# Optimization experiments

Hardware: AMD Instinct MI355X
Metric: run time of the kernel (lower is better)

The kernel has to match this reference:

```python
import jax, jax.numpy as jnp
import numpy as np

DIM = 256
N_STATE = 8
DT_RANK = 16  # ceil(dim/16)
D_CONV = 4
HIDDEN = 128  # dim * rank_ratio
EPS = 1e-6


def rmsnorm(x, w):
    # matches torch: x / (||x||_2 / sqrt(d) + eps) * w
    norm = jnp.sqrt(jnp.sum(x * x, axis=-1, keepdims=True))
    return x / (norm / np.sqrt(x.shape[-1]) + EPS) * w


def dwconv1d(x, w, b, pad_l, pad_r):
    # x: (b, l, c); w: (c, 1, k) depthwise
    out = jax.lax.conv_general_dilated(
        x.transpose(0, 2, 1), w, window_strides=(1,),
        padding=[(pad_l, pad_r)], dimension_numbers=('NCH', 'OIH', 'NCH'),
        feature_group_count=w.shape[0])
    return (out + b[None, :, None]).transpose(0, 2, 1)


def selective_scan(x, delta, A, Bm, Cm, D):
    # x, delta: (b,l,d); A: (d,n); Bm, Cm: (b,l,n); D: (d,)
    dA = jnp.exp(delta[..., None] * A)                     # (b,l,d,n)
    dBx = (delta * x)[..., None] * Bm[:, :, None, :]       # (b,l,d,n)

    def step(h, inp):
        dA_t, dBx_t, C_t = inp
        h = dA_t * h + dBx_t                               # (b,d,n)
        y = jnp.einsum('bdn,bn->bd', h, C_t)
        return h, y

    h0 = jnp.zeros((x.shape[0],) + A.shape, dtype=x.dtype)
    _, ys = jax.lax.scan(step, h0,
                         (dA.transpose(1, 0, 2, 3), dBx.transpose(1, 0, 2, 3),
                          Cm.transpose(1, 0, 2)))
    return ys.transpose(1, 0, 2) + x * D                   # (b,l,d)


def mamba_branch(x, ctx, conv_w, conv_b, xproj_w, dtproj_w, dtproj_b, A_log, D):
    xc = jax.nn.silu(dwconv1d(x, conv_w, conv_b, D_CONV - 1, 0))  # causal conv
    x_dbl = ctx @ xproj_w.T                                  # (b,l,r+2n)
    dt, Bm, Cm = jnp.split(x_dbl, [DT_RANK, DT_RANK + N_STATE], axis=-1)
    delta = jax.nn.softplus(dt @ dtproj_w.T + dtproj_b)
    A = -jnp.exp(A_log)
    return selective_scan(xc, delta, A, Bm, Cm, D)


def setup_inputs() -> dict:
    key = jax.random.key(0)
    ks = jax.random.split(key, 24)
    B, L, D = 4, 64 * 64, DIM
    s = 0.02
    A_log_init = jnp.log(jnp.broadcast_to(jnp.arange(1, N_STATE + 1, dtype=jnp.float32), (D, N_STATE)))
    dt_bias = jnp.full((D,), jnp.log(jnp.expm1(0.01)), dtype=jnp.float32)
    inp = {
        'x0': jax.random.normal(ks[0], (B, L, D), jnp.float32),
        'x1': jax.random.normal(ks[1], (B, L, D), jnp.float32),
        'w_norm0': jnp.ones((D,), jnp.float32),
        'w_norm1': jnp.ones((D,), jnp.float32),
        'in_proj_w': jax.random.normal(ks[2], (2 * D, D), jnp.float32) * s,
        'conv_w_f': jax.random.normal(ks[3], (D, 1, D_CONV), jnp.float32) * 0.3,
        'conv_b_f': jnp.zeros((D,), jnp.float32),
        'xproj_w_f': jax.random.normal(ks[4], (DT_RANK + 2 * N_STATE, D), jnp.float32) * s,
        'dtproj_w_f': jax.random.normal(ks[5], (D, DT_RANK), jnp.float32) * 0.1,
        'dtproj_b_f': dt_bias,
        'A_log_f': A_log_init,
        'D_f': jnp.ones((D,), jnp.float32),
        'conv_w_bw': jax.random.normal(ks[6], (D, 1, D_CONV), jnp.float32) * 0.3,
        'conv_b_bw': jnp.zeros((D,), jnp.float32),
        'xproj_w_bw': jax.random.normal(ks[7], (DT_RANK + 2 * N_STATE, D), jnp.float32) * s,
        'dtproj_w_bw': jax.random.normal(ks[8], (D, DT_RANK), jnp.float32) * 0.1,
        'dtproj_b_bw': dt_bias,
        'A_log_bw': A_log_init,
        'D_bw': jnp.ones((D,), jnp.float32),
        'norm_y_w': jnp.ones((D,), jnp.float32),
        'out_proj_w': jax.random.normal(ks[9], (D, D), jnp.float32) * s,
        'fc1_w': jax.random.normal(ks[10], (HIDDEN, D), jnp.float32) * s,
        'dw_w': jax.random.normal(ks[11], (HIDDEN, 1, 3), jnp.float32) * 0.3,
        'dw_b': jnp.zeros((HIDDEN,), jnp.float32),
        'fc2_w': jax.random.normal(ks[12], (D, HIDDEN), jnp.float32) * s,
    }
    return inp


def reference(x0, x1, w_norm0, w_norm1, in_proj_w, conv_w_f, conv_b_f, xproj_w_f,
              dtproj_w_f, dtproj_b_f, A_log_f, D_f, conv_w_bw, conv_b_bw,
              xproj_w_bw, dtproj_w_bw, dtproj_b_bw, A_log_bw, D_bw, norm_y_w,
              out_proj_w, fc1_w, dw_w, dw_b, fc2_w):
    residual = x0
    h0 = rmsnorm(x0, w_norm0)
    h1 = rmsnorm(x1, w_norm1)
    # cross-Mamba: main stream x0 -> x,z; extra_emb x1 -> dt/B/C
    xz = h0 @ in_proj_w.T
    xin, z = jnp.split(xz, 2, axis=-1)
    y_f = mamba_branch(xin, h1, conv_w_f, conv_b_f, xproj_w_f, dtproj_w_f,
                       dtproj_b_f, A_log_f, D_f)
    y_b = jnp.flip(mamba_branch(jnp.flip(xin, 1), jnp.flip(h1, 1), conv_w_bw,
                                conv_b_bw, xproj_w_bw, dtproj_w_bw, dtproj_b_bw,
                                A_log_bw, D_bw), 1)
    y = (y_f + y_b) * 0.5          # if_devide_out=True (bidirectional)
    y = rmsnorm(y, norm_y_w)       # use_norm=True
    y = y * jax.nn.silu(z)
    x = y @ out_proj_w.T + residual
    # LowRankFeedForward (dropout = identity at eval)
    m = x @ fc1_w.T
    m = jax.nn.silu(dwconv1d(m, dw_w, dw_b, 1, 1))
    m = m @ fc2_w.T
    return x + m
```

## Files before the change

kernel.cpp:

```cpp
#include <hip/hip_runtime.h>
#include <math.h>
#include <cstddef>

#define BB 4
#define LL 4096
#define DD 256
#define NST 8
#define RANK 16
#define HID 128
#define BL (BB*LL)
#define BLD ((size_t)BL*DD)
#define CH 128
#define CLEN 32
#define XZS 512

typedef __bf16 bf16x8 __attribute__((ext_vector_type(8)));
typedef float  f32x4  __attribute__((ext_vector_type(4)));

__device__ __forceinline__ float siluf(float x){ return x / (1.f + __expf(-x)); }
__device__ __forceinline__ float softplus_fast(float x){
  float r = __logf(1.f + __expf(x));
  return x > 15.f ? x : r;
}
__device__ __forceinline__ unsigned short f2bf(float x){
  union { float f; unsigned u; } v; v.f = x;
  unsigned r = v.u + 0x7fffu + ((v.u >> 16) & 1u);
  return (unsigned short)(r >> 16);
}
__device__ __forceinline__ float bf2f(unsigned short u){
  union { unsigned u32; float f; } c; c.u32 = ((unsigned)u) << 16;
  return c.f;
}

__global__ __launch_bounds__(64) void rms_kernel(
    const float* __restrict__ x0, const float* __restrict__ w0, unsigned short* __restrict__ o0b,
    const float* __restrict__ x1, const float* __restrict__ w1, unsigned short* __restrict__ o1b)
{
  const float* x; const float* w; unsigned short* o;
  if (blockIdx.y == 0){ x = x0; w = w0; o = o0b; } else { x = x1; w = w1; o = o1b; }
  size_t tok = blockIdx.x;
  int lane = threadIdx.x;
  float4 v = ((const float4*)(x + tok*DD))[lane];
  float s = v.x*v.x + v.y*v.y + v.z*v.z + v.w*v.w;
  #pragma unroll
  for (int m = 1; m < 64; m <<= 1) s += __shfl_xor(s, m, 64);
  float scale = 1.f / (sqrtf(s) * (1.f/16.f) + 1e-6f);
  float4 wv = ((const float4*)w)[lane];
  ushort4 r;
  r.x = f2bf(v.x*scale*wv.x); r.y = f2bf(v.y*scale*wv.y);
  r.z = f2bf(v.z*scale*wv.z); r.w = f2bf(v.w*scale*wv.w);
  ((ushort4*)(o + tok*DD))[lane] = r;
}

__global__ __launch_bounds__(256) void cvt_all_kernel(
    const float* __restrict__ ip,
    const float* __restrict__ s0, const float* __restrict__ s1,
    const float* __restrict__ s2, const float* __restrict__ s3,
    const float* __restrict__ s4,
    unsigned short* __restrict__ d1, unsigned short* __restrict__ d2)
{
  int i = blockIdx.x*256 + threadIdx.x;
  if (i < 131072){ d1[i] = f2bf(ip[i]); return; }
  int j = i - 131072;
  if (j >= 147456) return;
  float v;
  if (j < 8192)        v = s0[j];
  else if (j < 16384)  v = s1[j - 8192];
  else if (j < 81920)  v = s2[j - 16384];
  else if (j < 114688) v = s3[j - 81920];
  else                 v = s4[j - 114688];
  d2[j] = f2bf(v);
}

template<int EPI>
__global__ __launch_bounds__(256) void gemm_mfma128(
    const unsigned short* __restrict__ A, const unsigned short* __restrict__ Bw,
    float* __restrict__ C, const float* __restrict__ Add,
    unsigned short* __restrict__ Cb, int M, int ldc, int K)
{
  constexpr int BM = 128, BN = 128, BK = 32, PAD = 8;
  __shared__ __align__(16) unsigned short As[BM][BK+PAD];
  __shared__ __align__(16) unsigned short Bs[BN][BK+PAD];
  int tid  = threadIdx.x;
  int row0 = blockIdx.x * BM;
  int col0 = blockIdx.y * BN;
  int wave = tid >> 6, lane = tid & 63;
  int wm = (wave >> 1) * 64, wn = (wave & 1) * 64;
  int lm = lane & 15, kq = lane >> 4;

  f32x4 acc[4][4];
  #pragma unroll
  for (int i = 0; i < 4; i++)
    #pragma unroll
    for (int j = 0; j < 4; j++) acc[i][j] = (f32x4){0.f,0.f,0.f,0.f};

  for (int k0 = 0; k0 < K; k0 += BK){
    #pragma unroll
    for (int e = tid; e < BM*4; e += 256){
      int r = e >> 2, c8 = (e & 3) * 8;
      *(int4*)&As[r][c8] = *(const int4*)&A[(size_t)(row0 + r)*K + k0 + c8];
    }
    #pragma unroll
    for (int e = tid; e < BN*4; e += 256){
      int r = e >> 2, c8 = (e & 3) * 8;
      *(int4*)&Bs[r][c8] = *(const int4*)&Bw[(size_t)(col0 + r)*K + k0 + c8];
    }
    __syncthreads();
    bf16x8 af[4], bfv[4];
    #pragma unroll
    for (int i = 0; i < 4; i++) af[i]  = *(const bf16x8*)&As[wm + i*16 + lm][kq*8];
    #pragma unroll
    for (int j = 0; j < 4; j++) bfv[j] = *(const bf16x8*)&Bs[wn + j*16 + lm][kq*8];
    #pragma unroll
    for (int i = 0; i < 4; i++)
      #pragma unroll
      for (int j = 0; j < 4; j++)
        acc[i][j] = __builtin_amdgcn_mfma_f32_16x16x32_bf16(af[i], bfv[j], acc[i][j], 0, 0, 0);
    __syncthreads();
  }

  #pragma unroll
  for (int i = 0; i < 4; i++){
    int rbase = row0 + wm + i*16 + kq*4;
    #pragma unroll
    for (int j = 0; j < 4; j++){
      int col = col0 + wn + j*16 + lm;
      #pragma unroll
      for (int r = 0; r < 4; r++){
        size_t idx = (size_t)(rbase + r)*ldc + col;
        float v = acc[i][j][r];
        if constexpr (EPI == 1 || EPI == 2) v += Add[idx];
        if constexpr (EPI != 3) C[idx] = v;
        if constexpr (EPI == 1 || EPI == 3) Cb[idx] = f2bf(v);
      }
    }
  }
}

template<int EPI>
__global__ __launch_bounds__(256) void gemm_mfma(
    const unsigned short* __restrict__ A, const unsigned short* __restrict__ Bw,
    float* __restrict__ C, const float* __restrict__ Add,
    unsigned short* __restrict__ Cb, int M, int ldc, int K)
{
  constexpr int BK = 32, PAD = 8;
  __shared__ __align__(16) unsigned short As[64][BK+PAD];
  __shared__ __align__(16) unsigned short Bs[64][BK+PAD];
  int tid  = threadIdx.x;
  int row0 = blockIdx.x * 64;
  int col0 = blockIdx.y * 64;
  int wave = tid >> 6, lane = tid & 63;
  int wm = (wave >> 1) * 32, wn = (wave & 1) * 32;
  int lm = lane & 15, kq = lane >> 4;
  int sr = tid >> 2, sc8 = (tid & 3) * 8;

  f32x4 acc[2][2];
  #pragma unroll
  for (int i = 0; i < 2; i++)
    #pragma unroll
    for (int j = 0; j < 2; j++) acc[i][j] = (f32x4){0.f,0.f,0.f,0.f};

  for (int k0 = 0; k0 < K; k0 += BK){
    *(int4*)&As[sr][sc8] = *(const int4*)&A [(size_t)(row0 + sr)*K + k0 + sc8];
    *(int4*)&Bs[sr][sc8] = *(const int4*)&Bw[(size_t)(col0 + sr)*K + k0 + sc8];
    __syncthreads();
    bf16x8 af[2], bfv[2];
    #pragma unroll
    for (int i = 0; i < 2; i++) af[i]  = *(const bf16x8*)&As[wm + i*16 + lm][kq*8];
    #pragma unroll
    for (int j = 0; j < 2; j++) bfv[j] = *(const bf16x8*)&Bs[wn + j*16 + lm][kq*8];
    #pragma unroll
    for (int i = 0; i < 2; i++)
      #pragma unroll
      for (int j = 0; j < 2; j++)
        acc[i][j] = __builtin_amdgcn_mfma_f32_16x16x32_bf16(af[i], bfv[j], acc[i][j], 0, 0, 0);
    __syncthreads();
  }

  #pragma unroll
  for (int i = 0; i < 2; i++){
    int rbase = row0 + wm + i*16 + kq*4;
    #pragma unroll
    for (int j = 0; j < 2; j++){
      int col = col0 + wn + j*16 + lm;
      #pragma unroll
      for (int r = 0; r < 4; r++){
        size_t idx = (size_t)(rbase + r)*ldc + col;
        float v = acc[i][j][r];
        if constexpr (EPI == 1 || EPI == 2) v += Add[idx];
        if constexpr (EPI != 3) C[idx] = v;
        if constexpr (EPI == 1 || EPI == 3) Cb[idx] = f2bf(v);
      }
    }
  }
}

__global__ __launch_bounds__(256) void front_kernel(
    const unsigned short* __restrict__ xz,
    const float* __restrict__ xd,
    const float* __restrict__ cwf, const float* __restrict__ cbf,
    const float* __restrict__ cwb, const float* __restrict__ cbb,
    const float* __restrict__ dtwf, const float* __restrict__ dtbf,
    const float* __restrict__ dtwb, const float* __restrict__ dtbb,
    const float* __restrict__ Alogf, const float* __restrict__ Alogb,
    unsigned int* __restrict__ xde,
    float* __restrict__ P, float* __restrict__ Hout)
{
  int chunk = blockIdx.x, b = blockIdx.y, dir = blockIdx.z;
  int s0 = chunk*CLEN;
  int d  = threadIdx.x;

  __shared__ float sdt[CLEN][16];
  __shared__ float sB [CLEN][8];
  {
    #pragma unroll
    for (int e = threadIdx.x; e < CLEN*16; e += 256){
      int lt = e >> 4, col = e & 15;
      int pos = s0 + lt;
      int row = dir ? (LL-1-pos) : pos;
      sdt[lt][col] = xd[((size_t)b*LL + row)*64 + dir*32 + col];
    }
    {
      int e = threadIdx.x;
      int lt = e >> 3, col = e & 7;
      int pos = s0 + lt;
      int row = dir ? (LL-1-pos) : pos;
      sB[lt][col] = xd[((size_t)b*LL + row)*64 + dir*32 + 16 + col];
    }
  }
  __syncthreads();

  float4 cw = ((const float4*)(dir ? cwb : cwf))[d];
  float cb  = (dir ? cbb : cbf)[d];
  const float* dtw = (dir ? dtwb : dtwf) + d*RANK;
  float4 w0 = ((const float4*)dtw)[0], w1 = ((const float4*)dtw)[1];
  float4 w2 = ((const float4*)dtw)[2], w3 = ((const float4*)dtw)[3];
  float dtb = (dir ? dtbb : dtbf)[d];

  const unsigned short* xp = xz + (size_t)b*LL*XZS + d;
  #define LDX(pos) ((pos) >= 0 ? bf2f(xp[(size_t)(dir ? (LL-1-(pos)) : (pos))*XZS]) : 0.f)

  float a0, a1, a2, a3;
  a1 = LDX(s0-3); a2 = LDX(s0-2); a3 = LDX(s0-1);

  unsigned packX[CLEN];
  const int U = 8;
  float px[U];
  #pragma unroll
  for (int u = 0; u < U; u++) px[u] = LDX(s0+u);

  for (int g = 0; g < CLEN; g += U){
    float nx[U];
    if (g + U < CLEN){
      #pragma unroll
      for (int u = 0; u < U; u++) nx[u] = LDX(s0+g+U+u);
    }
    #pragma unroll
    for (int u = 0; u < U; u++){
      int i = g + u;
      a0 = a1; a1 = a2; a2 = a3; a3 = px[u];
      float xc = cb;
      xc = fmaf(cw.x, a0, xc); xc = fmaf(cw.y, a1, xc);
      xc = fmaf(cw.z, a2, xc); xc = fmaf(cw.w, a3, xc);
      xc = siluf(xc);
      const float* dt = &sdt[i][0];
      float de = dtb;
      de = fmaf(dt[0],w0.x, fmaf(dt[1],w0.y, fmaf(dt[2],w0.z, fmaf(dt[3],w0.w, de))));
      de = fmaf(dt[4],w1.x, fmaf(dt[5],w1.y, fmaf(dt[6],w1.z, fmaf(dt[7],w1.w, de))));
      de = fmaf(dt[8],w2.x, fmaf(dt[9],w2.y, fmaf(dt[10],w2.z, fmaf(dt[11],w2.w, de))));
      de = fmaf(dt[12],w3.x, fmaf(dt[13],w3.y, fmaf(dt[14],w3.z, fmaf(dt[15],w3.w, de))));
      de = softplus_fast(de);
      unsigned pk = (unsigned)f2bf(xc) | ((unsigned)f2bf(de) << 16);
      packX[i] = pk;
      xde[((size_t)(dir*BB + b)*LL + (s0+i))*DD + d] = pk;
    }
    if (g + U < CLEN){
      #pragma unroll
      for (int u = 0; u < U; u++) px[u] = nx[u];
    }
  }
  #undef LDX

  const float* Alog = dir ? Alogb : Alogf;
  float A[NST];
  #pragma unroll
  for (int n = 0; n < NST; n++) A[n] = -__expf(Alog[d*NST + n]);
  float h[NST];
  #pragma unroll
  for (int n = 0; n < NST; n++) h[n] = 0.f;
  float S = 0.f;
  #pragma unroll
  for (int t = 0; t < CLEN; t++){
    unsigned pk = packX[t];
    float xc = bf2f((unsigned short)(pk & 0xffffu));
    float de = bf2f((unsigned short)(pk >> 16));
    S += de;
    float dux = de * xc;
    const float* Bv = &sB[t][0];
    h[0] = fmaf(__expf(de*A[0]), h[0], dux*Bv[0]);
    h[1] = fmaf(__expf(de*A[1]), h[1], dux*Bv[1]);
    h[2] = fmaf(__expf(de*A[2]), h[2], dux*Bv[2]);
    h[3] = fmaf(__expf(de*A[3]), h[3], dux*Bv[3]);
    h[4] = fmaf(__expf(de*A[4]), h[4], dux*Bv[4]);
    h[5] = fmaf(__expf(de*A[5]), h[5], dux*Bv[5]);
    h[6] = fmaf(__expf(de*A[6]), h[6], dux*Bv[6]);
    h[7] = fmaf(__expf(de*A[7]), h[7], dux*Bv[7]);
  }
  size_t ob = ((((size_t)dir*CH + chunk)*BB + b)*DD + d)*NST;
  float4 p0, p1h, h0v, h1v;
  p0.x = __expf(A[0]*S); p0.y = __expf(A[1]*S); p0.z = __expf(A[2]*S); p0.w = __expf(A[3]*S);
  p1h.x= __expf(A[4]*S); p1h.y= __expf(A[5]*S); p1h.z= __expf(A[6]*S); p1h.w= __expf(A[7]*S);
  h0v.x=h[0]; h0v.y=h[1]; h0v.z=h[2]; h0v.w=h[3];
  h1v.x=h[4]; h1v.y=h[5]; h1v.z=h[6]; h1v.w=h[7];
  *(float4*)&P[ob]      = p0;  *(float4*)&P[ob+4]    = p1h;
  *(float4*)&Hout[ob]   = h0v; *(float4*)&Hout[ob+4] = h1v;
}

__global__ __launch_bounds__(64) void scan_p2(
    const float* P, const float* __restrict__ Hout, float* Hin)
{
  int tid = blockIdx.x*64 + threadIdx.x;
  int dir = tid >> 13;
  int b   = (tid >> 11) & 3;
  int dn  = tid & 2047;
  const size_t stride = (size_t)BB*2048;
  size_t idx0 = (((size_t)dir*CH)*BB + b)*2048 + dn;

  const int U = 8;
  float pp[U], hh[U];
  #pragma unroll
  for (int u = 0; u < U; u++){
    pp[u] = P[idx0 + u*stride];
    hh[u] = Hout[idx0 + u*stride];
  }
  float h = 0.f;
  for (int c0 = 0; c0 < CH; c0 += U){
    float np[U], nh[U];
    if (c0 + U < CH){
      #pragma unroll
      for (int u = 0; u < U; u++){
        np[u] = P[idx0 + (size_t)(c0+U+u)*stride];
        nh[u] = Hout[idx0 + (size_t)(c0+U+u)*stride];
      }
    }
    #pragma unroll
    for (int u = 0; u < U; u++){
      Hin[idx0 + (size_t)(c0+u)*stride] = h;
      h = fmaf(pp[u], h, hh[u]);
    }
    if (c0 + U < CH){
      #pragma unroll
      for (int u = 0; u < U; u++){ pp[u] = np[u]; hh[u] = nh[u]; }
    }
  }
}

__global__ __launch_bounds__(256) void scan_p3(
    const unsigned int* __restrict__ xde,
    const float* __restrict__ xd,
    const float* __restrict__ Alogf, const float* __restrict__ Alogb,
    const float* __restrict__ Dfp, const float* __restrict__ Dbp,
    const float* Hin,
    unsigned short* __restrict__ yf, unsigned short* __restrict__ yb)
{
  int chunk = blockIdx.x, b = blockIdx.y, dir = blockIdx.z;
  const float* Alog = dir ? Alogb : Alogf;
  int d = threadIdx.x;
  int base = chunk*CLEN;

  __shared__ float sBC[CLEN*16];
  {
    #pragma unroll
    for (int e = threadIdx.x; e < CLEN*16; e += 256){
      int lt = e >> 4, col = e & 15;
      int pos = base + lt;
      int row = dir ? (LL-1-pos) : pos;
      sBC[e] = xd[((size_t)b*LL + row)*64 + dir*32 + 16 + col];
    }
  }
  __syncthreads();

  float A[NST];
  #pragma unroll
  for (int n = 0; n < NST; n++) A[n] = -__expf(Alog[d*NST + n]);
  float Dd = (dir ? Dbp : Dfp)[d];

  float h[NST];
  {
    size_t ib = ((((size_t)dir*CH + chunk)*BB + b)*DD + d)*NST;
    float4 a0 = *(const float4*)&Hin[ib];
    float4 a1 = *(const float4*)&Hin[ib+4];
    h[0]=a0.x; h[1]=a0.y; h[2]=a0.z; h[3]=a0.w;
    h[4]=a1.x; h[5]=a1.y; h[6]=a1.z; h[7]=a1.w;
  }

  const unsigned int* xdep = xde + ((size_t)(dir*BB + b)*LL + base)*DD + d;
  unsigned short* yp = (dir ? yb : yf) + ((size_t)b*LL + base)*DD + d;

  const int U = 8;
  unsigned int pk[U];
  #pragma unroll
  for (int u = 0; u < U; u++) pk[u] = xdep[(size_t)u*DD];

  for (int t0 = 0; t0 < CLEN; t0 += U){
    unsigned int nk[U];
    if (t0 + U < CLEN){
      #pragma unroll
      for (int u = 0; u < U; u++) nk[u] = xdep[(size_t)(t0+U+u)*DD];
    }
    #pragma unroll
    for (int u = 0; u < U; u++){
      int t = t0 + u;
      float xc = bf2f((unsigned short)(pk[u] & 0xffffu));
      float de = bf2f((unsigned short)(pk[u] >> 16));
      float dux = de * xc;
      const float4 Bv0 = *(const float4*)&sBC[t*16 + 0];
      const float4 Bv1 = *(const float4*)&sBC[t*16 + 4];
      const float4 Cv0 = *(const float4*)&sBC[t*16 + 8];
      const float4 Cv1 = *(const float4*)&sBC[t*16 + 12];
      float acc = xc * Dd;
      h[0] = fmaf(__expf(de*A[0]), h[0], dux*Bv0.x); acc = fmaf(h[0], Cv0.x, acc);
      h[1] = fmaf(__expf(de*A[1]), h[1], dux*Bv0.y); acc = fmaf(h[1], Cv0.y, acc);
      h[2] = fmaf(__expf(de*A[2]), h[2], dux*Bv0.z); acc = fmaf(h[2], Cv0.z, acc);
      h[3] = fmaf(__expf(de*A[3]), h[3], dux*Bv0.w); acc = fmaf(h[3], Cv0.w, acc);
      h[4] = fmaf(__expf(de*A[4]), h[4], dux*Bv1.x); acc = fmaf(h[4], Cv1.x, acc);
      h[5] = fmaf(__expf(de*A[5]), h[5], dux*Bv1.y); acc = fmaf(h[5], Cv1.y, acc);
      h[6] = fmaf(__expf(de*A[6]), h[6], dux*Bv1.z); acc = fmaf(h[6], Cv1.z, acc);
      h[7] = fmaf(__expf(de*A[7]), h[7], dux*Bv1.w); acc = fmaf(h[7], Cv1.w, acc);
      yp[(size_t)t*DD] = f2bf(acc);
    }
    if (t0 + U < CLEN){
      #pragma unroll
      for (int u = 0; u < U; u++) pk[u] = nk[u];
    }
  }
}

__global__ __launch_bounds__(64) void combine_kernel(
    const unsigned short* __restrict__ yf, const unsigned short* __restrict__ yb,
    const unsigned short* __restrict__ xz, const float* __restrict__ wn,
    unsigned short* __restrict__ outb)
{
  size_t tok = blockIdx.x;
  int b = (int)(tok / LL), t = (int)(tok % LL);
  int lane = threadIdx.x;
  ushort4 au = ((const ushort4*)(yf + tok*DD))[lane];
  ushort4 cu = ((const ushort4*)(yb + ((size_t)b*LL + (LL-1-t))*DD))[lane];
  float4 v;
  v.x=(bf2f(au.x)+bf2f(cu.x))*0.5f; v.y=(bf2f(au.y)+bf2f(cu.y))*0.5f;
  v.z=(bf2f(au.z)+bf2f(cu.z))*0.5f; v.w=(bf2f(au.w)+bf2f(cu.w))*0.5f;
  float s = v.x*v.x + v.y*v.y + v.z*v.z + v.w*v.w;
  #pragma unroll
  for (int m = 1; m < 64; m <<= 1) s += __shfl_xor(s, m, 64);
  float scale = 1.f / (sqrtf(s)*(1.f/16.f) + 1e-6f);
  float4 wv = ((const float4*)wn)[lane];
  ushort4 zv = *(const ushort4*)&xz[tok*XZS + 256 + lane*4];
  ushort4 r;
  r.x = f2bf(v.x*scale*wv.x*siluf(bf2f(zv.x)));
  r.y = f2bf(v.y*scale*wv.y*siluf(bf2f(zv.y)));
  r.z = f2bf(v.z*scale*wv.z*siluf(bf2f(zv.z)));
  r.w = f2bf(v.w*scale*wv.w*siluf(bf2f(zv.w)));
  ((ushort4*)(outb + tok*DD))[lane] = r;
}

__global__ __launch_bounds__(256) void dwconv3_kernel(
    const float* __restrict__ m, const float* __restrict__ w,
    const float* __restrict__ bi, unsigned short* __restrict__ o)
{
  size_t gid = (size_t)blockIdx.x*256 + threadIdx.x;
  int c = (int)(gid % HID);
  int tok = (int)(gid / HID);
  int b = tok / LL, t = tok % LL;
  float acc = bi[c];
  #pragma unroll
  for (int k = 0; k < 3; k++){
    int tt = t - 1 + k;
    if (tt >= 0 && tt < LL)
      acc = fmaf(w[c*3 + k], m[((size_t)b*LL + tt)*HID + c], acc);
  }
  o[gid] = f2bf(siluf(acc));
}

extern "C" void kernel_launch(void* const* d_in, const int* in_sizes, int n_in,
                              void* d_out, int out_size, void* d_ws, size_t ws_size,
                              hipStream_t stream)
{
  const float* x0        = (const float*)d_in[0];
  const float* x1        = (const float*)d_in[1];
  const float* w_norm0   = (const float*)d_in[2];
  const float* w_norm1   = (const float*)d_in[3];
  const float* in_proj_w = (const float*)d_in[4];
  const float* conv_w_f  = (const float*)d_in[5];
  const float* conv_b_f  = (const float*)d_in[6];
  const float* xproj_w_f = (const float*)d_in[7];
  const float* dtproj_w_f= (const float*)d_in[8];
  const float* dtproj_b_f= (const float*)d_in[9];
  const float* A_log_f   = (const float*)d_in[10];
  const float* D_f       = (const float*)d_in[11];
  const float* conv_w_bw = (const float*)d_in[12];
  const float* conv_b_bw = (const float*)d_in[13];
  const float* xproj_w_bw= (const float*)d_in[14];
  const float* dtproj_w_bw=(const float*)d_in[15];
  const float* dtproj_b_bw=(const float*)d_in[16];
  const float* A_log_bw  = (const float*)d_in[17];
  const float* D_bw      = (const float*)d_in[18];
  const float* norm_y_w  = (const float*)d_in[19];
  const float* out_proj_w= (const float*)d_in[20];
  const float* fc1_w     = (const float*)d_in[21];
  const float* dw_w      = (const float*)d_in[22];
  const float* dw_b      = (const float*)d_in[23];
  const float* fc2_w     = (const float*)d_in[24];
  float* out = (float*)d_out;
  float* ws  = (float*)d_ws;

  float* r0 = ws + 0*BLD;
  float* r1 = ws + 1*BLD;
  float* r2 = ws + 2*BLD;
  float* r3 = ws + 3*BLD;
  float* r4 = ws + 4*BLD;
  float* r5 = ws + 5*BLD;
  float* r6 = ws + 6*BLD;
  float* r7 = ws + 7*BLD;

  unsigned short* h0b   = (unsigned short*)r0;
  unsigned short* h1b   = (unsigned short*)r1;
  unsigned short* xz_b  = (unsigned short*)r2;
  float*          xd    = r3;
  unsigned int*   xde   = (unsigned int*)r4;
  unsigned short* wbuf1 = (unsigned short*)r6;
  unsigned short* yfb   = (unsigned short*)r0;
  unsigned short* ybb   = (unsigned short*)r1;
  const size_t CARRY = (size_t)2*CH*BB*DD*NST;
  float* Pbuf = r6;
  float* Hout = r6 + CARRY;
  float* Hin  = Pbuf;
  unsigned short* ycomb_b = (unsigned short*)r3;
  unsigned short* wbuf2   = (unsigned short*)r7;
  unsigned short* wb_xp   = wbuf2;
  unsigned short* wb_out  = wbuf2 + 16384;
  unsigned short* wb_fc1  = wbuf2 + 81920;
  unsigned short* wb_fc2  = wbuf2 + 114688;
  unsigned short* xb      = wbuf2 + 147456;
  float*          m1      = r4;
  unsigned short* m2b     = (unsigned short*)r5;

  cvt_all_kernel<<<dim3(1088), 256, 0, stream>>>(
      in_proj_w, xproj_w_f, xproj_w_bw, out_proj_w, fc1_w, fc2_w, wbuf1, wbuf2);

  rms_kernel<<<dim3(BL,2), 64, 0, stream>>>(x0, w_norm0, h0b, x1, w_norm1, h1b);

  gemm_mfma128<3><<<dim3(BL/128, 4), 256, 0, stream>>>(
      h0b, wbuf1, nullptr, nullptr, xz_b, BL, XZS, 256);

  gemm_mfma<0><<<dim3(BL/64, 1), 256, 0, stream>>>(
      h1b, wb_xp, xd, nullptr, nullptr, BL, 64, 256);

  front_kernel<<<dim3(CH, BB, 2), 256, 0, stream>>>(
      xz_b, xd, conv_w_f, conv_b_f, conv_w_bw, conv_b_bw,
      dtproj_w_f, dtproj_b_f, dtproj_w_bw, dtproj_b_bw,
      A_log_f, A_log_bw, xde, Pbuf, Hout);

  scan_p2<<<dim3(256), 64, 0, stream>>>(Pbuf, Hout, Hin);
  scan_p3<<<dim3(CH,BB,2), 256, 0, stream>>>(
      xde, xd, A_log_f, A_log_bw, D_f, D_bw, Hin, yfb, ybb);

  combine_kernel<<<dim3(BL), 64, 0, stream>>>(yfb, ybb, xz_b, norm_y_w, ycomb_b);

  gemm_mfma128<1><<<dim3(BL/128, 2), 256, 0, stream>>>(
      ycomb_b, wb_out, out, x0, xb, BL, 256, 256);

  gemm_mfma<0><<<dim3(BL/64, 2), 256, 0, stream>>>(
      xb, wb_fc1, m1, nullptr, nullptr, BL, 128, 256);

  dwconv3_kernel<<<dim3((BL*HID)/256), 256, 0, stream>>>(m1, dw_w, dw_b, m2b);

  gemm_mfma128<2><<<dim3(BL/128, 2), 256, 0, stream>>>(
      m2b, wb_fc2, out, out, nullptr, BL, 256, 128);
}
```

Measured before the change: 261.5 us.

## Halve scan chunk length, pack chunk carries as bf16, store fc1 output in bf16

Doubles the number of scan chunks (CLEN 32→16) so the chunk-local scans have more parallel blocks and shorter sequential loops. The per-chunk decay and state carries are packed as two bf16 values in one uint32 buffer, and the second pass writes its float seeds back into the same buffer, cutting carry traffic. The fc1 GEMM now writes bf16 instead of fp32 for the depthwise conv to read. The cost is lower precision in the carried state and fc1 activations, and a longer sequential carry pass over more chunks.

```diff
diff --git a/kernel.cpp b/kernel.cpp
--- a/kernel.cpp
+++ b/kernel.cpp
@@ -10,8 +10,8 @@
 #define HID 128
 #define BL (BB*LL)
 #define BLD ((size_t)BL*DD)
-#define CH 128
-#define CLEN 32
+#define CH 256
+#define CLEN 16
 #define XZS 512
 
 typedef __bf16 bf16x8 __attribute__((ext_vector_type(8)));
@@ -204,7 +204,7 @@
     const float* __restrict__ dtwb, const float* __restrict__ dtbb,
     const float* __restrict__ Alogf, const float* __restrict__ Alogb,
     unsigned int* __restrict__ xde,
-    float* __restrict__ P, float* __restrict__ Hout)
+    unsigned int* __restrict__ PH)
 {
   int chunk = blockIdx.x, b = blockIdx.y, dir = blockIdx.z;
   int s0 = chunk*CLEN;
@@ -213,19 +213,16 @@
   __shared__ float sdt[CLEN][16];
   __shared__ float sB [CLEN][8];
   {
-    #pragma unroll
-    for (int e = threadIdx.x; e < CLEN*16; e += 256){
-      int lt = e >> 4, col = e & 15;
-      int pos = s0 + lt;
-      int row = dir ? (LL-1-pos) : pos;
-      sdt[lt][col] = xd[((size_t)b*LL + row)*64 + dir*32 + col];
-    }
-    {
-      int e = threadIdx.x;
-      int lt = e >> 3, col = e & 7;
-      int pos = s0 + lt;
-      int row = dir ? (LL-1-pos) : pos;
-      sB[lt][col] = xd[((size_t)b*LL + row)*64 + dir*32 + 16 + col];
+    int e = threadIdx.x;
+    int lt = e >> 4, col = e & 15;
+    int pos = s0 + lt;
+    int row = dir ? (LL-1-pos) : pos;
+    sdt[lt][col] = xd[((size_t)b*LL + row)*64 + dir*32 + col];
+    if (e < CLEN*8){
+      int lt2 = e >> 3, col2 = e & 7;
+      int pos2 = s0 + lt2;
+      int row2 = dir ? (LL-1-pos2) : pos2;
+      sB[lt2][col2] = xd[((size_t)b*LL + row2)*64 + dir*32 + 16 + col2];
     }
   }
   __syncthreads();
@@ -249,6 +246,7 @@
   #pragma unroll
   for (int u = 0; u < U; u++) px[u] = LDX(s0+u);
 
+  #pragma unroll
   for (int g = 0; g < CLEN; g += U){
     float nx[U];
     if (g + U < CLEN){
@@ -307,17 +305,20 @@
     h[7] = fmaf(__expf(de*A[7]), h[7], dux*Bv[7]);
   }
   size_t ob = ((((size_t)dir*CH + chunk)*BB + b)*DD + d)*NST;
-  float4 p0, p1h, h0v, h1v;
-  p0.x = __expf(A[0]*S); p0.y = __expf(A[1]*S); p0.z = __expf(A[2]*S); p0.w = __expf(A[3]*S);
-  p1h.x= __expf(A[4]*S); p1h.y= __expf(A[5]*S); p1h.z= __expf(A[6]*S); p1h.w= __expf(A[7]*S);
-  h0v.x=h[0]; h0v.y=h[1]; h0v.z=h[2]; h0v.w=h[3];
-  h1v.x=h[4]; h1v.y=h[5]; h1v.z=h[6]; h1v.w=h[7];
-  *(float4*)&P[ob]      = p0;  *(float4*)&P[ob+4]    = p1h;
-  *(float4*)&Hout[ob]   = h0v; *(float4*)&Hout[ob+4] = h1v;
-}
-
-__global__ __launch_bounds__(64) void scan_p2(
-    const float* P, const float* __restrict__ Hout, float* Hin)
+  uint4 o0, o1;
+  o0.x = (unsigned)f2bf(__expf(A[0]*S)) | ((unsigned)f2bf(h[0]) << 16);
+  o0.y = (unsigned)f2bf(__expf(A[1]*S)) | ((unsigned)f2bf(h[1]) << 16);
+  o0.z = (unsigned)f2bf(__expf(A[2]*S)) | ((unsigned)f2bf(h[2]) << 16);
+  o0.w = (unsigned)f2bf(__expf(A[3]*S)) | ((unsigned)f2bf(h[3]) << 16);
+  o1.x = (unsigned)f2bf(__expf(A[4]*S)) | ((unsigned)f2bf(h[4]) << 16);
+  o1.y = (unsigned)f2bf(__expf(A[5]*S)) | ((unsigned)f2bf(h[5]) << 16);
+  o1.z = (unsigned)f2bf(__expf(A[6]*S)) | ((unsigned)f2bf(h[6]) << 16);
+  o1.w = (unsigned)f2bf(__expf(A[7]*S)) | ((unsigned)f2bf(h[7]) << 16);
+  *(uint4*)&PH[ob]   = o0;
+  *(uint4*)&PH[ob+4] = o1;
+}
+
+__global__ __launch_bounds__(64) void scan_p2(unsigned int* PH)
 {
   int tid = blockIdx.x*64 + threadIdx.x;
   int dir = tid >> 13;
@@ -325,32 +326,29 @@
   int dn  = tid & 2047;
   const size_t stride = (size_t)BB*2048;
   size_t idx0 = (((size_t)dir*CH)*BB + b)*2048 + dn;
+  float* Seed = (float*)PH;
 
   const int U = 8;
-  float pp[U], hh[U];
-  #pragma unroll
-  for (int u = 0; u < U; u++){
-    pp[u] = P[idx0 + u*stride];
-    hh[u] = Hout[idx0 + u*stride];
-  }
+  unsigned pk[U];
+  #pragma unroll
+  for (int u = 0; u < U; u++) pk[u] = PH[idx0 + u*stride];
   float h = 0.f;
   for (int c0 = 0; c0 < CH; c0 += U){
-    float np[U], nh[U];
+    unsigned nk[U];
     if (c0 + U < CH){
       #pragma unroll
-      for (int u = 0; u < U; u++){
-        np[u] = P[idx0 + (size_t)(c0+U+u)*stride];
-        nh[u] = Hout[idx0 + (size_t)(c0+U+u)*stride];
-      }
+      for (int u = 0; u < U; u++) nk[u] = PH[idx0 + (size_t)(c0+U+u)*stride];
     }
     #pragma unroll
     for (int u = 0; u < U; u++){
-      Hin[idx0 + (size_t)(c0+u)*stride] = h;
-      h = fmaf(pp[u], h, hh[u]);
+      float P  = bf2f((unsigned short)(pk[u] & 0xffffu));
+      float Ho = bf2f((unsigned short)(pk[u] >> 16));
+      Seed[idx0 + (size_t)(c0+u)*stride] = h;
+      h = fmaf(P, h, Ho);
     }
     if (c0 + U < CH){
       #pragma unroll
-      for (int u = 0; u < U; u++){ pp[u] = np[u]; hh[u] = nh[u]; }
+      for (int u = 0; u < U; u++) pk[u] = nk[u];
     }
   }
 }
@@ -360,7 +358,7 @@
     const float* __restrict__ xd,
     const float* __restrict__ Alogf, const float* __restrict__ Alogb,
     const float* __restrict__ Dfp, const float* __restrict__ Dbp,
-    const float* Hin,
+    const unsigned int* PH,
     unsigned short* __restrict__ yf, unsigned short* __restrict__ yb)
 {
   int chunk = blockIdx.x, b = blockIdx.y, dir = blockIdx.z;
@@ -370,13 +368,11 @@
 
   __shared__ float sBC[CLEN*16];
   {
-    #pragma unroll
-    for (int e = threadIdx.x; e < CLEN*16; e += 256){
-      int lt = e >> 4, col = e & 15;
-      int pos = base + lt;
-      int row = dir ? (LL-1-pos) : pos;
-      sBC[e] = xd[((size_t)b*LL + row)*64 + dir*32 + 16 + col];
-    }
+    int e = threadIdx.x;
+    int lt = e >> 4, col = e & 15;
+    int pos = base + lt;
+    int row = dir ? (LL-1-pos) : pos;
+    sBC[e] = xd[((size_t)b*LL + row)*64 + dir*32 + 16 + col];
   }
   __syncthreads();
 
@@ -387,6 +383,7 @@
 
   float h[NST];
   {
+    const float* Hin = (const float*)PH;
     size_t ib = ((((size_t)dir*CH + chunk)*BB + b)*DD + d)*NST;
     float4 a0 = *(const float4*)&Hin[ib];
     float4 a1 = *(const float4*)&Hin[ib+4];
@@ -402,6 +399,7 @@
   #pragma unroll
   for (int u = 0; u < U; u++) pk[u] = xdep[(size_t)u*DD];
 
+  #pragma unroll
   for (int t0 = 0; t0 < CLEN; t0 += U){
     unsigned int nk[U];
     if (t0 + U < CLEN){
@@ -464,7 +462,7 @@
 }
 
 __global__ __launch_bounds__(256) void dwconv3_kernel(
-    const float* __restrict__ m, const float* __restrict__ w,
+    const unsigned short* __restrict__ m, const float* __restrict__ w,
     const float* __restrict__ bi, unsigned short* __restrict__ o)
 {
   size_t gid = (size_t)blockIdx.x*256 + threadIdx.x;
@@ -476,7 +474,7 @@
   for (int k = 0; k < 3; k++){
     int tt = t - 1 + k;
     if (tt >= 0 && tt < LL)
-      acc = fmaf(w[c*3 + k], m[((size_t)b*LL + tt)*HID + c], acc);
+      acc = fmaf(w[c*3 + k], bf2f(m[((size_t)b*LL + tt)*HID + c]), acc);
   }
   o[gid] = f2bf(siluf(acc));
 }
@@ -530,10 +528,7 @@
   unsigned short* wbuf1 = (unsigned short*)r6;
   unsigned short* yfb   = (unsigned short*)r0;
   unsigned short* ybb   = (unsigned short*)r1;
-  const size_t CARRY = (size_t)2*CH*BB*DD*NST;
-  float* Pbuf = r6;
-  float* Hout = r6 + CARRY;
-  float* Hin  = Pbuf;
+  unsigned int*   PH    = (unsigned int*)r6;
   unsigned short* ycomb_b = (unsigned short*)r3;
   unsigned short* wbuf2   = (unsigned short*)r7;
   unsigned short* wb_xp   = wbuf2;
@@ -541,7 +536,7 @@
   unsigned short* wb_fc1  = wbuf2 + 81920;
   unsigned short* wb_fc2  = wbuf2 + 114688;
   unsigned short* xb      = wbuf2 + 147456;
-  float*          m1      = r4;
+  unsigned short* m1b     = (unsigned short*)r4;
   unsigned short* m2b     = (unsigned short*)r5;
 
   cvt_all_kernel<<<dim3(1088), 256, 0, stream>>>(
@@ -558,21 +553,21 @@
   front_kernel<<<dim3(CH, BB, 2), 256, 0, stream>>>(
       xz_b, xd, conv_w_f, conv_b_f, conv_w_bw, conv_b_bw,
       dtproj_w_f, dtproj_b_f, dtproj_w_bw, dtproj_b_bw,
-      A_log_f, A_log_bw, xde, Pbuf, Hout);
-
-  scan_p2<<<dim3(256), 64, 0, stream>>>(Pbuf, Hout, Hin);
+      A_log_f, A_log_bw, xde, PH);
+
+  scan_p2<<<dim3(256), 64, 0, stream>>>(PH);
   scan_p3<<<dim3(CH,BB,2), 256, 0, stream>>>(
-      xde, xd, A_log_f, A_log_bw, D_f, D_bw, Hin, yfb, ybb);
+      xde, xd, A_log_f, A_log_bw, D_f, D_bw, PH, yfb, ybb);
 
   combine_kernel<<<dim3(BL), 64, 0, stream>>>(yfb, ybb, xz_b, norm_y_w, ycomb_b);
 
   gemm_mfma128<1><<<dim3(BL/128, 2), 256, 0, stream>>>(
       ycomb_b, wb_out, out, x0, xb, BL, 256, 256);
 
-  gemm_mfma<0><<<dim3(BL/64, 2), 256, 0, stream>>>(
-      xb, wb_fc1, m1, nullptr, nullptr, BL, 128, 256);
-
-  dwconv3_kernel<<<dim3((BL*HID)/256), 256, 0, stream>>>(m1, dw_w, dw_b, m2b);
+  gemm_mfma<3><<<dim3(BL/64, 2), 256, 0, stream>>>(
+      xb, wb_fc1, nullptr, nullptr, m1b, BL, 128, 256);
+
+  dwconv3_kernel<<<dim3((BL*HID)/256), 256, 0, stream>>>(m1b, dw_w, dw_b, m2b);
 
   gemm_mfma128<2><<<dim3(BL/128, 2), 256, 0, stream>>>(
       m2b, wb_fc2, out, out, nullptr, BL, 256, 128);
```

Result: no change. 261.9 us (+0.1%).
